# Performance work log

Measured on AMD Instinct MI355X. Metric: run time of the kernel, lower is better.

Reference implementation:

```python
import jax, jax.numpy as jnp
import numpy as np

N = 50000        # nodes
E = 100000       # directed edges
F_NODE = 22      # atom features
F_EDGE = 4       # bond features
H = 64           # hidden_dim
EPS = 1e-5       # BatchNorm eps


def setup_inputs() -> dict:
    key = jax.random.key(0)
    ks = jax.random.split(key, 16)
    s = 0.05
    return {
        "x": jax.random.normal(ks[0], (N, F_NODE), dtype=jnp.float32),
        "edge_attr": jax.random.normal(ks[1], (E, F_EDGE), dtype=jnp.float32),
        "We1": jax.random.normal(ks[2], (F_EDGE, F_NODE * H), dtype=jnp.float32) * s,
        "be1": jnp.zeros((F_NODE * H,), dtype=jnp.float32),
        "root1": jax.random.normal(ks[3], (F_NODE, H), dtype=jnp.float32) * s,
        "b1": jnp.zeros((H,), dtype=jnp.float32),
        "g1": jnp.ones((H,), dtype=jnp.float32),
        "beta1": jnp.zeros((H,), dtype=jnp.float32),
        "We2": jax.random.normal(ks[4], (F_EDGE, H * H), dtype=jnp.float32) * s,
        "be2": jnp.zeros((H * H,), dtype=jnp.float32),
        "root2": jax.random.normal(ks[5], (H, H), dtype=jnp.float32) * s,
        "b2": jnp.zeros((H,), dtype=jnp.float32),
        "g2": jnp.ones((H,), dtype=jnp.float32),
        "beta2": jnp.zeros((H,), dtype=jnp.float32),
        "Wfc": jax.random.normal(ks[6], (H, 1), dtype=jnp.float32) * s,
        "bfc": jnp.zeros((1,), dtype=jnp.float32),
        "edge_index": jax.random.randint(ks[7], (2, E), 0, N, dtype=jnp.int32),
    }


def nnconv(x, edge_index, edge_attr, We, be, root, bias, in_ch, out_ch):
    # PyG NNConv (aggr='add', root_weight=True):
    #   out_i = x_i @ root + bias + sum_{(j->i)} x_j @ reshape(MLP(e_ji), [in, out])
    src, dst = edge_index[0], edge_index[1]
    w = jax.nn.relu(edge_attr @ We + be).reshape(-1, in_ch, out_ch)  # [E, in, out]
    msg = jnp.einsum('ei,eio->eo', x[src], w)                        # [E, out]
    agg = jax.ops.segment_sum(msg, dst, num_segments=x.shape[0])     # [N, out]
    return agg + x @ root + bias


def batchnorm(x, gamma, beta):
    # training-mode BatchNorm1d: batch statistics, biased variance
    mu = jnp.mean(x, axis=0)
    var = jnp.mean(jnp.square(x - mu), axis=0)
    return (x - mu) * jax.lax.rsqrt(var + EPS) * gamma + beta


def reference(x, edge_attr, We1, be1, root1, b1, g1, beta1,
              We2, be2, root2, b2, g2, beta2, Wfc, bfc, edge_index):
    h = nnconv(x, edge_index, edge_attr, We1, be1, root1, b1, F_NODE, H)
    h = jax.nn.relu(batchnorm(h, g1, beta1))
    # dropout is identity in eval / deterministic reference
    h = nnconv(h, edge_index, edge_attr, We2, be2, root2, b2, H, H)
    h = jax.nn.relu(batchnorm(h, g2, beta2))
    return jax.nn.sigmoid(h @ Wfc + bfc)  # [N, 1]
```

## Files before the change

### kernel.cpp

```cpp
#include <hip/hip_runtime.h>
#include <math.h>

#define N_NODES 50000
#define N_EDGES 100000
#define FNODE 22
#define HDIM 64
#define BN_EPS 1e-5f

typedef __attribute__((ext_vector_type(8))) short bfrag;
typedef __attribute__((ext_vector_type(4))) float facc;
typedef __attribute__((ext_vector_type(4))) unsigned int uint4v;
typedef __attribute__((ext_vector_type(2))) unsigned int uint2v;

__device__ __forceinline__ unsigned f2bf(float x) {
    unsigned u = __float_as_uint(x);
    return (u + 0x7FFFu + ((u >> 16) & 1u)) >> 16;
}
__device__ __forceinline__ unsigned pk2bf(float lo, float hi) {
    return f2bf(lo) | (f2bf(hi) << 16);
}
__device__ __forceinline__ float bflo(unsigned w) { return __uint_as_float(w << 16); }
__device__ __forceinline__ float bfhi(unsigned w) { return __uint_as_float(w & 0xFFFF0000u); }

__global__ void k_packX(const float* __restrict__ x, unsigned* __restrict__ xbf) {
    int idx = blockIdx.x * 256 + threadIdx.x;
    if (idx < N_NODES * 12) {
        int n = idx / 12, c2 = idx - n * 12;
        int c = c2 * 2;
        float lo = (c < FNODE) ? x[n * FNODE + c] : 0.f;
        float hi = (c + 1 < FNODE) ? x[n * FNODE + c + 1] : 0.f;
        xbf[idx] = pk2bf(lo, hi);
    }
}

template <int K>
__global__ void k_packB(const float* __restrict__ W, uint4v* __restrict__ Bt) {
    constexpr int NQ = (K + 31) / 32;
    int t = threadIdx.x;
    int ot = t >> 6, lane = t & 63;
    int o = ot * 16 + (lane & 15);
    int kg = lane >> 4;
#pragma unroll
    for (int q = 0; q < NQ; ++q) {
        unsigned w[4];
#pragma unroll
        for (int p = 0; p < 4; ++p) {
            int k0 = q * 32 + kg * 8 + 2 * p;
            float lo = (k0 < K) ? W[k0 * HDIM + o] : 0.f;
            float hi = (k0 + 1 < K) ? W[(k0 + 1) * HDIM + o] : 0.f;
            w[p] = pk2bf(lo, hi);
        }
        Bt[(ot * NQ + q) * 64 + lane] = uint4v{w[0], w[1], w[2], w[3]};
    }
}

__global__ void k_node1(const float* __restrict__ x, const uint4v* __restrict__ Bt1,
                        const float* __restrict__ b1, float* __restrict__ h1) {
    int lane = threadIdx.x & 63;
    int m = lane & 15, kg = lane >> 4, orow4 = kg * 4;
    int tile = blockIdx.x * 4 + (threadIdx.x >> 6);
    int nb = tile * 16;
    if (nb >= N_NODES) return;
    const float* xr = x + (size_t)(nb + m) * FNODE;
    float xv[8];
#pragma unroll
    for (int p = 0; p < 4; ++p) {
        int c = kg * 8 + 2 * p;
        float2 v = (c + 1 < FNODE) ? *(const float2*)(xr + c) : float2{0.f, 0.f};
        xv[2 * p] = v.x; xv[2 * p + 1] = v.y;
    }
    bfrag A = __builtin_bit_cast(bfrag, uint4v{pk2bf(xv[0], xv[1]), pk2bf(xv[2], xv[3]),
                                               pk2bf(xv[4], xv[5]), pk2bf(xv[6], xv[7])});
    const facc zero4 = {0.f, 0.f, 0.f, 0.f};
#pragma unroll
    for (int ot = 0; ot < 4; ++ot) {
        bfrag B = __builtin_bit_cast(bfrag, Bt1[ot * 64 + lane]);
        facc d = __builtin_amdgcn_mfma_f32_16x16x32_bf16(A, B, zero4, 0, 0, 0);
        float bv = b1[ot * 16 + m];
#pragma unroll
        for (int j = 0; j < 4; ++j)
            h1[(size_t)(nb + orow4 + j) * HDIM + ot * 16 + m] = d[j] + bv;
    }
}

__launch_bounds__(256, 4)
__global__ void k_edge1(const char* __restrict__ hrows, const float* __restrict__ ea,
                        const float* __restrict__ We, const float* __restrict__ be,
                        const int* __restrict__ eidx, float* __restrict__ out) {
    constexpr int IN = FNODE;
    constexpr int INH = IN * HDIM;
    __shared__ uint4v Wf[IN * HDIM];
    __shared__ float hsl[4][16 * 28];

    for (int idx = threadIdx.x; idx < IN * HDIM; idx += 256) {
        int i = idx >> 6, o = idx & 63;
        int c = i * HDIM + o;
        Wf[idx] = uint4v{pk2bf(We[c], We[INH + c]),
                         pk2bf(We[2 * INH + c], We[3 * INH + c]),
                         f2bf(be[c]), 0u};
    }
    __syncthreads();

    int lane = threadIdx.x & 63;
    int e16 = lane & 15;
    int orow4 = (lane >> 4) * 4;
    int tile = blockIdx.x * 4 + (threadIdx.x >> 6);
    int ebase = tile * 16;
    if (ebase >= N_EDGES) return;
    float* hs = &hsl[threadIdx.x >> 6][0];

    bool act = lane < 16;
    float4 ea0 = ((const float4*)ea)[ebase + e16];
    unsigned aone = act ? 0x3F80u : 0u;
    bfrag A0 = __builtin_bit_cast(bfrag, uint4v{act ? pk2bf(ea0.x, ea0.y) : 0u,
                                                act ? pk2bf(ea0.z, ea0.w) : 0u, aone, 0u});

    if (lane < 48) {
        int r = lane / 3, c16 = lane - r * 3;
        int src = eidx[ebase + r];
        uint4v hv = *(const uint4v*)(hrows + (size_t)src * 48 + c16 * 16);
        *(float4*)&hs[r * 28 + c16 * 8] =
            float4{bflo(hv.x), bfhi(hv.x), bflo(hv.y), bfhi(hv.y)};
        *(float4*)&hs[r * 28 + c16 * 8 + 4] =
            float4{bflo(hv.z), bfhi(hv.z), bflo(hv.w), bfhi(hv.w)};
    }

    const facc zero4 = {0.f, 0.f, 0.f, 0.f};
    facc m0[4] = {zero4, zero4, zero4, zero4};

#pragma unroll
    for (int i0 = 0; i0 < 20; i0 += 4) {
        float4 hA[4];
#pragma unroll
        for (int j = 0; j < 4; ++j)
            hA[j] = *(const float4*)&hs[(orow4 + j) * 28 + i0];
#pragma unroll
        for (int di = 0; di < 4; ++di) {
#pragma unroll
            for (int t = 0; t < 4; ++t) {
                bfrag B = __builtin_bit_cast(bfrag, Wf[(i0 + di) * 64 + t * 16 + e16]);
                facc t0 = __builtin_amdgcn_mfma_f32_16x16x32_bf16(A0, B, zero4, 0, 0, 0);
#pragma unroll
                for (int j = 0; j < 4; ++j)
                    m0[t][j] = fmaf((&hA[j].x)[di], fmaxf(t0[j], 0.f), m0[t][j]);
            }
        }
    }
    {
        float4 hA[4];
#pragma unroll
        for (int j = 0; j < 4; ++j)
            hA[j] = *(const float4*)&hs[(orow4 + j) * 28 + 20];
#pragma unroll
        for (int di = 0; di < 2; ++di) {
#pragma unroll
            for (int t = 0; t < 4; ++t) {
                bfrag B = __builtin_bit_cast(bfrag, Wf[(20 + di) * 64 + t * 16 + e16]);
                facc t0 = __builtin_amdgcn_mfma_f32_16x16x32_bf16(A0, B, zero4, 0, 0, 0);
#pragma unroll
                for (int j = 0; j < 4; ++j)
                    m0[t][j] = fmaf((&hA[j].x)[di], fmaxf(t0[j], 0.f), m0[t][j]);
            }
        }
    }

    int dA[4];
#pragma unroll
    for (int j = 0; j < 4; ++j)
        dA[j] = eidx[N_EDGES + ebase + orow4 + j];
#pragma unroll
    for (int t = 0; t < 4; ++t) {
#pragma unroll
        for (int j = 0; j < 4; ++j)
            atomicAdd(&out[(size_t)dA[j] * HDIM + t * 16 + e16], m0[t][j]);
    }
}

__launch_bounds__(256, 3)
__global__ void k_edge2(const char* __restrict__ hrows, const float* __restrict__ ea,
                        const float* __restrict__ We, const float* __restrict__ be,
                        const int* __restrict__ eidx, float* __restrict__ out) {
    constexpr int IN = HDIM;
    constexpr int INH = IN * HDIM;
    constexpr int SSTRIDE = 36;
    __shared__ uint4v Wf[IN * 32];
    __shared__ unsigned hsl[4][32 * SSTRIDE];

    int obeg = (blockIdx.x & 1) * 32;
    int tileblk = blockIdx.x >> 1;

    for (int idx = threadIdx.x; idx < IN * 32; idx += 256) {
        int i = idx >> 5, oloc = idx & 31;
        int c = i * HDIM + obeg + oloc;
        Wf[idx] = uint4v{pk2bf(We[c], We[INH + c]),
                         pk2bf(We[2 * INH + c], We[3 * INH + c]),
                         f2bf(be[c]), 0u};
    }
    __syncthreads();

    int lane = threadIdx.x & 63;
    int e16 = lane & 15;
    int orow4 = (lane >> 4) * 4;
    int tile = tileblk * 4 + (threadIdx.x >> 6);
    int ebase = tile * 32;
    if (ebase >= N_EDGES) return;
    unsigned* hs = &hsl[threadIdx.x >> 6][0];

    bool act = lane < 16;
    float4 ea0 = ((const float4*)ea)[ebase + e16];
    float4 ea1 = ((const float4*)ea)[ebase + 16 + e16];
    unsigned aone = act ? 0x3F80u : 0u;
    bfrag A0 = __builtin_bit_cast(bfrag, uint4v{act ? pk2bf(ea0.x, ea0.y) : 0u,
                                                act ? pk2bf(ea0.z, ea0.w) : 0u, aone, 0u});
    bfrag A1 = __builtin_bit_cast(bfrag, uint4v{act ? pk2bf(ea1.x, ea1.y) : 0u,
                                                act ? pk2bf(ea1.z, ea1.w) : 0u, aone, 0u});

#pragma unroll
    for (int p = 0; p < 4; ++p) {
        int idx = p * 64 + lane;
        int r = idx >> 3, c16 = idx & 7;
        int src = eidx[ebase + r];
        uint4v hv = *(const uint4v*)(hrows + (size_t)src * 128 + c16 * 16);
        *(uint4v*)&hs[r * SSTRIDE + c16 * 4] = hv;
    }

    const facc zero4 = {0.f, 0.f, 0.f, 0.f};
    facc m0[2] = {zero4, zero4}, m1[2] = {zero4, zero4};

#pragma unroll
    for (int i0 = 0; i0 < IN; i0 += 4) {
        float hA[4][4], hB[4][4];
#pragma unroll
        for (int j = 0; j < 4; ++j) {
            uint2v wA = *(const uint2v*)&hs[(orow4 + j) * SSTRIDE + i0 / 2];
            hA[j][0] = bflo(wA.x); hA[j][1] = bfhi(wA.x);
            hA[j][2] = bflo(wA.y); hA[j][3] = bfhi(wA.y);
            uint2v wB = *(const uint2v*)&hs[(16 + orow4 + j) * SSTRIDE + i0 / 2];
            hB[j][0] = bflo(wB.x); hB[j][1] = bfhi(wB.x);
            hB[j][2] = bflo(wB.y); hB[j][3] = bfhi(wB.y);
        }
#pragma unroll
        for (int di = 0; di < 4; ++di) {
#pragma unroll
            for (int t = 0; t < 2; ++t) {
                bfrag B = __builtin_bit_cast(bfrag, Wf[(i0 + di) * 32 + t * 16 + e16]);
                facc t0 = __builtin_amdgcn_mfma_f32_16x16x32_bf16(A0, B, zero4, 0, 0, 0);
                facc t1 = __builtin_amdgcn_mfma_f32_16x16x32_bf16(A1, B, zero4, 0, 0, 0);
#pragma unroll
                for (int j = 0; j < 4; ++j) {
                    m0[t][j] = fmaf(hA[j][di], fmaxf(t0[j], 0.f), m0[t][j]);
                    m1[t][j] = fmaf(hB[j][di], fmaxf(t1[j], 0.f), m1[t][j]);
                }
            }
        }
    }

    int dA[4], dB[4];
#pragma unroll
    for (int j = 0; j < 4; ++j) {
        dA[j] = eidx[N_EDGES + ebase + orow4 + j];
        dB[j] = eidx[N_EDGES + ebase + 16 + orow4 + j];
    }
#pragma unroll
    for (int t = 0; t < 2; ++t) {
#pragma unroll
        for (int j = 0; j < 4; ++j) {
            atomicAdd(&out[(size_t)dA[j] * HDIM + obeg + t * 16 + e16], m0[t][j]);
            atomicAdd(&out[(size_t)dB[j] * HDIM + obeg + t * 16 + e16], m1[t][j]);
        }
    }
}

__global__ void k_stats(const float* __restrict__ hbuf, float* stats) {
    int c = threadIdx.x & 63;
    int r = threadIdx.x >> 6;
    int rowsPer = blockDim.x >> 6;
    float s = 0.f, q = 0.f;
    for (int n = blockIdx.x * rowsPer + r; n < N_NODES; n += gridDim.x * rowsPer) {
        float v = hbuf[n * HDIM + c];
        s += v;
        q = fmaf(v, v, q);
    }
    __shared__ float ls[4][64], lq[4][64];
    ls[r][c] = s;
    lq[r][c] = q;
    __syncthreads();
    if (r == 0) {
        s = ls[0][c] + ls[1][c] + ls[2][c] + ls[3][c];
        q = lq[0][c] + lq[1][c] + lq[2][c] + lq[3][c];
        atomicAdd(&stats[c], s);
        atomicAdd(&stats[64 + c], q);
    }
}

__global__ void k_finalize(const float* stats_in, const float* __restrict__ g,
                           const float* __restrict__ beta, float* as_out) {
    int c = threadIdx.x;
    float mu = stats_in[c] * (1.f / N_NODES);
    float var = stats_in[64 + c] * (1.f / N_NODES) - mu * mu;
    var = fmaxf(var, 0.f);
    float a = g[c] * rsqrtf(var + BN_EPS);
    as_out[c] = a;
    as_out[64 + c] = beta[c] - mu * a;
}

__global__ void k_apply1(const float* h1, const float* __restrict__ as1,
                         const uint4v* __restrict__ Bt, const float* __restrict__ b2,
                         unsigned* __restrict__ hbf, float* h2) {
    int lane = threadIdx.x & 63;
    int m = lane & 15, kg = lane >> 4, orow4 = (lane >> 4) * 4;
    int tile = blockIdx.x * 4 + (threadIdx.x >> 6);
    int nb = tile * 16;
    if (nb >= N_NODES) return;
    int node = nb + m;
    const float* hr = h1 + (size_t)node * HDIM;

    float4 a0 = *(const float4*)(as1 + kg * 8), a1 = *(const float4*)(as1 + kg * 8 + 4);
    float4 s0 = *(const float4*)(as1 + 64 + kg * 8), s1 = *(const float4*)(as1 + 64 + kg * 8 + 4);
    float4 a2 = *(const float4*)(as1 + 32 + kg * 8), a3 = *(const float4*)(as1 + 32 + kg * 8 + 4);
    float4 s2 = *(const float4*)(as1 + 96 + kg * 8), s3 = *(const float4*)(as1 + 96 + kg * 8 + 4);

    float4 v0 = *(const float4*)(hr + kg * 8), v1 = *(const float4*)(hr + kg * 8 + 4);
    float4 v2 = *(const float4*)(hr + 32 + kg * 8), v3 = *(const float4*)(hr + 32 + kg * 8 + 4);

    float r0[8], r1[8];
#pragma unroll
    for (int p = 0; p < 4; ++p) {
        r0[p]     = fmaxf(fmaf((&v0.x)[p], (&a0.x)[p], (&s0.x)[p]), 0.f);
        r0[p + 4] = fmaxf(fmaf((&v1.x)[p], (&a1.x)[p], (&s1.x)[p]), 0.f);
        r1[p]     = fmaxf(fmaf((&v2.x)[p], (&a2.x)[p], (&s2.x)[p]), 0.f);
        r1[p + 4] = fmaxf(fmaf((&v3.x)[p], (&a3.x)[p], (&s3.x)[p]), 0.f);
    }
    uint4v pk0 = uint4v{pk2bf(r0[0], r0[1]), pk2bf(r0[2], r0[3]),
                        pk2bf(r0[4], r0[5]), pk2bf(r0[6], r0[7])};
    uint4v pk1 = uint4v{pk2bf(r1[0], r1[1]), pk2bf(r1[2], r1[3]),
                        pk2bf(r1[4], r1[5]), pk2bf(r1[6], r1[7])};
    *(uint4v*)(hbf + (size_t)node * 32 + kg * 4)      = pk0;
    *(uint4v*)(hbf + (size_t)node * 32 + 16 + kg * 4) = pk1;

    bfrag A0 = __builtin_bit_cast(bfrag, pk0);
    bfrag A1 = __builtin_bit_cast(bfrag, pk1);

    const facc zero4 = {0.f, 0.f, 0.f, 0.f};
#pragma unroll
    for (int ot = 0; ot < 4; ++ot) {
        bfrag B0 = __builtin_bit_cast(bfrag, Bt[(ot * 2 + 0) * 64 + lane]);
        bfrag B1 = __builtin_bit_cast(bfrag, Bt[(ot * 2 + 1) * 64 + lane]);
        facc d = __builtin_amdgcn_mfma_f32_16x16x32_bf16(A0, B0, zero4, 0, 0, 0);
        d = __builtin_amdgcn_mfma_f32_16x16x32_bf16(A1, B1, d, 0, 0, 0);
        float bv = b2[ot * 16 + m];
#pragma unroll
        for (int j = 0; j < 4; ++j)
            h2[(size_t)(nb + orow4 + j) * HDIM + ot * 16 + m] = d[j] + bv;
    }
}

__global__ void k_final(const float* __restrict__ h2, const float* __restrict__ as2,
                        const float* __restrict__ Wfc, const float* __restrict__ bfc,
                        float* __restrict__ out) {
    int lane = threadIdx.x & 63;
    int n = blockIdx.x * (blockDim.x >> 6) + (threadIdx.x >> 6);
    if (n >= N_NODES) return;
    float a = as2[lane], s = as2[64 + lane];
    float v = fmaxf(fmaf(h2[n * HDIM + lane], a, s), 0.f) * Wfc[lane];
#pragma unroll
    for (int off = 32; off > 0; off >>= 1) v += __shfl_xor(v, off, 64);
    if (lane == 0) out[n] = 1.f / (1.f + expf(-(v + bfc[0])));
}

extern "C" void kernel_launch(void* const* d_in, const int* in_sizes, int n_in,
                              void* d_out, int out_size, void* d_ws, size_t ws_size,
                              hipStream_t stream) {
    const float* x     = (const float*)d_in[0];
    const float* ea    = (const float*)d_in[1];
    const float* We1   = (const float*)d_in[2];
    const float* be1   = (const float*)d_in[3];
    const float* root1 = (const float*)d_in[4];
    const float* b1    = (const float*)d_in[5];
    const float* g1    = (const float*)d_in[6];
    const float* beta1 = (const float*)d_in[7];
    const float* We2   = (const float*)d_in[8];
    const float* be2   = (const float*)d_in[9];
    const float* root2 = (const float*)d_in[10];
    const float* b2    = (const float*)d_in[11];
    const float* g2    = (const float*)d_in[12];
    const float* beta2 = (const float*)d_in[13];
    const float* Wfc   = (const float*)d_in[14];
    const float* bfc   = (const float*)d_in[15];
    const int*   eidx  = (const int*)d_in[16];
    float* out = (float*)d_out;

    char* ws = (char*)d_ws;
    size_t off = 0;
    auto alloc = [&](size_t bytes) { char* p = ws + off; off = (off + bytes + 255) & ~(size_t)255; return p; };
    float*    h1    = (float*)alloc((size_t)N_NODES * HDIM * 4);
    unsigned* hbf   = (unsigned*)alloc((size_t)N_NODES * 32 * 4);
    unsigned* xbf   = (unsigned*)alloc((size_t)N_NODES * 12 * 4);
    float*    stats = (float*)alloc(512 * 4);
    uint4v*   Bt2   = (uint4v*)alloc(8 * 64 * 16);
    uint4v*   Bt1   = (uint4v*)alloc(4 * 64 * 16);

    hipMemsetAsync(stats, 0, 512 * sizeof(float), stream);
    k_packX<<<(N_NODES * 12 + 255) / 256, 256, 0, stream>>>(x, xbf);
    k_packB<HDIM><<<1, 256, 0, stream>>>(root2, Bt2);
    k_packB<FNODE><<<1, 256, 0, stream>>>(root1, Bt1);

    const int e1Blocks = (N_EDGES / 16 + 3) / 4;
    const int e2Blocks = 2 * ((N_EDGES / 32 + 3) / 4);
    const int nodeBlocks = (N_NODES + 3) / 4;
    const int tileBlocks = (N_NODES / 16 + 3) / 4;

    k_node1<<<tileBlocks, 256, 0, stream>>>(x, Bt1, b1, h1);
    k_edge1<<<e1Blocks, 256, 0, stream>>>((const char*)xbf, ea, We1, be1, eidx, h1);
    k_stats<<<256, 256, 0, stream>>>(h1, stats);
    k_finalize<<<1, 64, 0, stream>>>(stats, g1, beta1, stats + 128);
    k_apply1<<<tileBlocks, 256, 0, stream>>>(h1, stats + 128, Bt2, b2, hbf, h1);
    k_edge2<<<e2Blocks, 256, 0, stream>>>((const char*)hbf, ea, We2, be2, eidx, h1);
    k_stats<<<256, 256, 0, stream>>>(h1, stats + 256);
    k_finalize<<<1, 64, 0, stream>>>(stats + 256, g2, beta2, stats + 384);
    k_final<<<nodeBlocks, 256, 0, stream>>>(h1, stats + 384, Wfc, bfc, out);
}
```

Before: 173.1 us.

## Merge prep kernels, fold BN finalize into stats, and rebalance edge kernels

The memset, X packing and both root-weight packing launches are combined into one k_prep kernel. The BN finalize step now runs inside k_stats through a last-block-done counter, which removes two launches. k_edge1 now splits output columns across two blocks, as k_edge2 already did, so each block holds half the weights in LDS. k_edge2 drops to 16 edges per wave and unpacks the gathered rows to fp32 in LDS, which trades per-wave work and LDS footprint against more blocks and twice the weight-staging loads.

Result: slower. 177.4 us (+2.5%).

```diff
diff --git a/kernel.cpp b/kernel.cpp
--- a/kernel.cpp
+++ b/kernel.cpp
@@ -6,11 +6,11 @@
 #define FNODE 22
 #define HDIM 64
 #define BN_EPS 1e-5f
+#define PXBLK ((N_NODES * 12 + 255) / 256)
 
 typedef __attribute__((ext_vector_type(8))) short bfrag;
 typedef __attribute__((ext_vector_type(4))) float facc;
 typedef __attribute__((ext_vector_type(4))) unsigned int uint4v;
-typedef __attribute__((ext_vector_type(2))) unsigned int uint2v;
 
 __device__ __forceinline__ unsigned f2bf(float x) {
     unsigned u = __float_as_uint(x);
@@ -22,28 +22,14 @@
 __device__ __forceinline__ float bflo(unsigned w) { return __uint_as_float(w << 16); }
 __device__ __forceinline__ float bfhi(unsigned w) { return __uint_as_float(w & 0xFFFF0000u); }
 
-__global__ void k_packX(const float* __restrict__ x, unsigned* __restrict__ xbf) {
-    int idx = blockIdx.x * 256 + threadIdx.x;
-    if (idx < N_NODES * 12) {
-        int n = idx / 12, c2 = idx - n * 12;
-        int c = c2 * 2;
-        float lo = (c < FNODE) ? x[n * FNODE + c] : 0.f;
-        float hi = (c + 1 < FNODE) ? x[n * FNODE + c + 1] : 0.f;
-        xbf[idx] = pk2bf(lo, hi);
-    }
-}
-
-template <int K>
-__global__ void k_packB(const float* __restrict__ W, uint4v* __restrict__ Bt) {
-    constexpr int NQ = (K + 31) / 32;
+__device__ __forceinline__ void packB_dev(const float* W, uint4v* Bt, int K) {
+    int NQ = (K + 31) / 32;
     int t = threadIdx.x;
     int ot = t >> 6, lane = t & 63;
     int o = ot * 16 + (lane & 15);
     int kg = lane >> 4;
-#pragma unroll
     for (int q = 0; q < NQ; ++q) {
         unsigned w[4];
-#pragma unroll
         for (int p = 0; p < 4; ++p) {
             int k0 = q * 32 + kg * 8 + 2 * p;
             float lo = (k0 < K) ? W[k0 * HDIM + o] : 0.f;
@@ -51,6 +37,30 @@
             w[p] = pk2bf(lo, hi);
         }
         Bt[(ot * NQ + q) * 64 + lane] = uint4v{w[0], w[1], w[2], w[3]};
+    }
+}
+
+__global__ void k_prep(const float* __restrict__ x, unsigned* __restrict__ xbf,
+                       const float* __restrict__ root1, const float* __restrict__ root2,
+                       uint4v* __restrict__ Bt1, uint4v* __restrict__ Bt2,
+                       float* __restrict__ stats, int* __restrict__ counters) {
+    int b = blockIdx.x;
+    if (b < PXBLK) {
+        int idx = b * 256 + threadIdx.x;
+        if (idx < N_NODES * 12) {
+            int n = idx / 12, c2 = idx - n * 12;
+            int c = c2 * 2;
+            float lo = (c < FNODE) ? x[n * FNODE + c] : 0.f;
+            float hi = (c + 1 < FNODE) ? x[n * FNODE + c + 1] : 0.f;
+            xbf[idx] = pk2bf(lo, hi);
+        }
+    } else if (b == PXBLK) {
+        packB_dev(root2, Bt2, HDIM);
+    } else if (b == PXBLK + 1) {
+        packB_dev(root1, Bt1, FNODE);
+    } else {
+        for (int idx = threadIdx.x; idx < 512; idx += 256) stats[idx] = 0.f;
+        if (threadIdx.x < 2) counters[threadIdx.x] = 0;
     }
 }
 
@@ -87,104 +97,9 @@
 __global__ void k_edge1(const char* __restrict__ hrows, const float* __restrict__ ea,
                         const float* __restrict__ We, const float* __restrict__ be,
                         const int* __restrict__ eidx, float* __restrict__ out) {
-    constexpr int IN = FNODE;
-    constexpr int INH = IN * HDIM;
-    __shared__ uint4v Wf[IN * HDIM];
-    __shared__ float hsl[4][16 * 28];
-
-    for (int idx = threadIdx.x; idx < IN * HDIM; idx += 256) {
-        int i = idx >> 6, o = idx & 63;
-        int c = i * HDIM + o;
-        Wf[idx] = uint4v{pk2bf(We[c], We[INH + c]),
-                         pk2bf(We[2 * INH + c], We[3 * INH + c]),
-                         f2bf(be[c]), 0u};
-    }
-    __syncthreads();
-
-    int lane = threadIdx.x & 63;
-    int e16 = lane & 15;
-    int orow4 = (lane >> 4) * 4;
-    int tile = blockIdx.x * 4 + (threadIdx.x >> 6);
-    int ebase = tile * 16;
-    if (ebase >= N_EDGES) return;
-    float* hs = &hsl[threadIdx.x >> 6][0];
-
-    bool act = lane < 16;
-    float4 ea0 = ((const float4*)ea)[ebase + e16];
-    unsigned aone = act ? 0x3F80u : 0u;
-    bfrag A0 = __builtin_bit_cast(bfrag, uint4v{act ? pk2bf(ea0.x, ea0.y) : 0u,
-                                                act ? pk2bf(ea0.z, ea0.w) : 0u, aone, 0u});
-
-    if (lane < 48) {
-        int r = lane / 3, c16 = lane - r * 3;
-        int src = eidx[ebase + r];
-        uint4v hv = *(const uint4v*)(hrows + (size_t)src * 48 + c16 * 16);
-        *(float4*)&hs[r * 28 + c16 * 8] =
-            float4{bflo(hv.x), bfhi(hv.x), bflo(hv.y), bfhi(hv.y)};
-        *(float4*)&hs[r * 28 + c16 * 8 + 4] =
-            float4{bflo(hv.z), bfhi(hv.z), bflo(hv.w), bfhi(hv.w)};
-    }
-
-    const facc zero4 = {0.f, 0.f, 0.f, 0.f};
-    facc m0[4] = {zero4, zero4, zero4, zero4};
-
-#pragma unroll
-    for (int i0 = 0; i0 < 20; i0 += 4) {
-        float4 hA[4];
-#pragma unroll
-        for (int j = 0; j < 4; ++j)
-            hA[j] = *(const float4*)&hs[(orow4 + j) * 28 + i0];
-#pragma unroll
-        for (int di = 0; di < 4; ++di) {
-#pragma unroll
-            for (int t = 0; t < 4; ++t) {
-                bfrag B = __builtin_bit_cast(bfrag, Wf[(i0 + di) * 64 + t * 16 + e16]);
-                facc t0 = __builtin_amdgcn_mfma_f32_16x16x32_bf16(A0, B, zero4, 0, 0, 0);
-#pragma unroll
-                for (int j = 0; j < 4; ++j)
-                    m0[t][j] = fmaf((&hA[j].x)[di], fmaxf(t0[j], 0.f), m0[t][j]);
-            }
-        }
-    }
-    {
-        float4 hA[4];
-#pragma unroll
-        for (int j = 0; j < 4; ++j)
-            hA[j] = *(const float4*)&hs[(orow4 + j) * 28 + 20];
-#pragma unroll
-        for (int di = 0; di < 2; ++di) {
-#pragma unroll
-            for (int t = 0; t < 4; ++t) {
-                bfrag B = __builtin_bit_cast(bfrag, Wf[(20 + di) * 64 + t * 16 + e16]);
-                facc t0 = __builtin_amdgcn_mfma_f32_16x16x32_bf16(A0, B, zero4, 0, 0, 0);
-#pragma unroll
-                for (int j = 0; j < 4; ++j)
-                    m0[t][j] = fmaf((&hA[j].x)[di], fmaxf(t0[j], 0.f), m0[t][j]);
-            }
-        }
-    }
-
-    int dA[4];
-#pragma unroll
-    for (int j = 0; j < 4; ++j)
-        dA[j] = eidx[N_EDGES + ebase + orow4 + j];
-#pragma unroll
-    for (int t = 0; t < 4; ++t) {
-#pragma unroll
-        for (int j = 0; j < 4; ++j)
-            atomicAdd(&out[(size_t)dA[j] * HDIM + t * 16 + e16], m0[t][j]);
-    }
-}
-
-__launch_bounds__(256, 3)
-__global__ void k_edge2(const char* __restrict__ hrows, const float* __restrict__ ea,
-                        const float* __restrict__ We, const float* __restrict__ be,
-                        const int* __restrict__ eidx, float* __restrict__ out) {
-    constexpr int IN = HDIM;
-    constexpr int INH = IN * HDIM;
-    constexpr int SSTRIDE = 36;
+    constexpr int IN = FNODE, INH = IN * HDIM, SSTRIDE = 28;
     __shared__ uint4v Wf[IN * 32];
-    __shared__ unsigned hsl[4][32 * SSTRIDE];
+    __shared__ float hsl[4][16 * SSTRIDE];
 
     int obeg = (blockIdx.x & 1) * 32;
     int tileblk = blockIdx.x >> 1;
@@ -202,82 +117,165 @@
     int e16 = lane & 15;
     int orow4 = (lane >> 4) * 4;
     int tile = tileblk * 4 + (threadIdx.x >> 6);
-    int ebase = tile * 32;
+    int ebase = tile * 16;
     if (ebase >= N_EDGES) return;
-    unsigned* hs = &hsl[threadIdx.x >> 6][0];
+    float* hs = &hsl[threadIdx.x >> 6][0];
 
     bool act = lane < 16;
     float4 ea0 = ((const float4*)ea)[ebase + e16];
-    float4 ea1 = ((const float4*)ea)[ebase + 16 + e16];
     unsigned aone = act ? 0x3F80u : 0u;
     bfrag A0 = __builtin_bit_cast(bfrag, uint4v{act ? pk2bf(ea0.x, ea0.y) : 0u,
                                                 act ? pk2bf(ea0.z, ea0.w) : 0u, aone, 0u});
-    bfrag A1 = __builtin_bit_cast(bfrag, uint4v{act ? pk2bf(ea1.x, ea1.y) : 0u,
-                                                act ? pk2bf(ea1.z, ea1.w) : 0u, aone, 0u});
-
-#pragma unroll
-    for (int p = 0; p < 4; ++p) {
+
+    if (lane < 48) {
+        int r = lane / 3, c16 = lane - r * 3;
+        int src = eidx[ebase + r];
+        uint4v hv = *(const uint4v*)(hrows + (size_t)src * 48 + c16 * 16);
+        *(float4*)&hs[r * SSTRIDE + c16 * 8] =
+            float4{bflo(hv.x), bfhi(hv.x), bflo(hv.y), bfhi(hv.y)};
+        *(float4*)&hs[r * SSTRIDE + c16 * 8 + 4] =
+            float4{bflo(hv.z), bfhi(hv.z), bflo(hv.w), bfhi(hv.w)};
+    }
+
+    const facc zero4 = {0.f, 0.f, 0.f, 0.f};
+    facc m0[2] = {zero4, zero4};
+
+#pragma unroll
+    for (int i0 = 0; i0 < 20; i0 += 4) {
+        float4 hA[4];
+#pragma unroll
+        for (int j = 0; j < 4; ++j)
+            hA[j] = *(const float4*)&hs[(orow4 + j) * SSTRIDE + i0];
+#pragma unroll
+        for (int di = 0; di < 4; ++di) {
+#pragma unroll
+            for (int t = 0; t < 2; ++t) {
+                bfrag B = __builtin_bit_cast(bfrag, Wf[(i0 + di) * 32 + t * 16 + e16]);
+                facc t0 = __builtin_amdgcn_mfma_f32_16x16x32_bf16(A0, B, zero4, 0, 0, 0);
+#pragma unroll
+                for (int j = 0; j < 4; ++j)
+                    m0[t][j] = fmaf((&hA[j].x)[di], fmaxf(t0[j], 0.f), m0[t][j]);
+            }
+        }
+    }
+    {
+        float4 hA[4];
+#pragma unroll
+        for (int j = 0; j < 4; ++j)
+            hA[j] = *(const float4*)&hs[(orow4 + j) * SSTRIDE + 20];
+#pragma unroll
+        for (int di = 0; di < 2; ++di) {
+#pragma unroll
+            for (int t = 0; t < 2; ++t) {
+                bfrag B = __builtin_bit_cast(bfrag, Wf[(20 + di) * 32 + t * 16 + e16]);
+                facc t0 = __builtin_amdgcn_mfma_f32_16x16x32_bf16(A0, B, zero4, 0, 0, 0);
+#pragma unroll
+                for (int j = 0; j < 4; ++j)
+                    m0[t][j] = fmaf((&hA[j].x)[di], fmaxf(t0[j], 0.f), m0[t][j]);
+            }
+        }
+    }
+
+    int dA[4];
+#pragma unroll
+    for (int j = 0; j < 4; ++j)
+        dA[j] = eidx[N_EDGES + ebase + orow4 + j];
+#pragma unroll
+    for (int t = 0; t < 2; ++t) {
+#pragma unroll
+        for (int j = 0; j < 4; ++j)
+            atomicAdd(&out[(size_t)dA[j] * HDIM + obeg + t * 16 + e16], m0[t][j]);
+    }
+}
+
+__launch_bounds__(256, 3)
+__global__ void k_edge2(const char* __restrict__ hrows, const float* __restrict__ ea,
+                        const float* __restrict__ We, const float* __restrict__ be,
+                        const int* __restrict__ eidx, float* __restrict__ out) {
+    constexpr int IN = HDIM, INH = IN * HDIM, SSTRIDE = 68;
+    __shared__ uint4v Wf[IN * 32];
+    __shared__ float hsl[4][16 * SSTRIDE];
+
+    int obeg = (blockIdx.x & 1) * 32;
+    int tileblk = blockIdx.x >> 1;
+
+    for (int idx = threadIdx.x; idx < IN * 32; idx += 256) {
+        int i = idx >> 5, oloc = idx & 31;
+        int c = i * HDIM + obeg + oloc;
+        Wf[idx] = uint4v{pk2bf(We[c], We[INH + c]),
+                         pk2bf(We[2 * INH + c], We[3 * INH + c]),
+                         f2bf(be[c]), 0u};
+    }
+    __syncthreads();
+
+    int lane = threadIdx.x & 63;
+    int e16 = lane & 15;
+    int orow4 = (lane >> 4) * 4;
+    int tile = tileblk * 4 + (threadIdx.x >> 6);
+    int ebase = tile * 16;
+    if (ebase >= N_EDGES) return;
+    float* hs = &hsl[threadIdx.x >> 6][0];
+
+    bool act = lane < 16;
+    float4 ea0 = ((const float4*)ea)[ebase + e16];
+    unsigned aone = act ? 0x3F80u : 0u;
+    bfrag A0 = __builtin_bit_cast(bfrag, uint4v{act ? pk2bf(ea0.x, ea0.y) : 0u,
+                                                act ? pk2bf(ea0.z, ea0.w) : 0u, aone, 0u});
+
+#pragma unroll
+    for (int p = 0; p < 2; ++p) {
         int idx = p * 64 + lane;
         int r = idx >> 3, c16 = idx & 7;
         int src = eidx[ebase + r];
         uint4v hv = *(const uint4v*)(hrows + (size_t)src * 128 + c16 * 16);
-        *(uint4v*)&hs[r * SSTRIDE + c16 * 4] = hv;
+        *(float4*)&hs[r * SSTRIDE + c16 * 8] =
+            float4{bflo(hv.x), bfhi(hv.x), bflo(hv.y), bfhi(hv.y)};
+        *(float4*)&hs[r * SSTRIDE + c16 * 8 + 4] =
+            float4{bflo(hv.z), bfhi(hv.z), bflo(hv.w), bfhi(hv.w)};
     }
 
     const facc zero4 = {0.f, 0.f, 0.f, 0.f};
-    facc m0[2] = {zero4, zero4}, m1[2] = {zero4, zero4};
+    facc m0[2] = {zero4, zero4};
 
 #pragma unroll
     for (int i0 = 0; i0 < IN; i0 += 4) {
-        float hA[4][4], hB[4][4];
-#pragma unroll
-        for (int j = 0; j < 4; ++j) {
-            uint2v wA = *(const uint2v*)&hs[(orow4 + j) * SSTRIDE + i0 / 2];
-            hA[j][0] = bflo(wA.x); hA[j][1] = bfhi(wA.x);
-            hA[j][2] = bflo(wA.y); hA[j][3] = bfhi(wA.y);
-            uint2v wB = *(const uint2v*)&hs[(16 + orow4 + j) * SSTRIDE + i0 / 2];
-            hB[j][0] = bflo(wB.x); hB[j][1] = bfhi(wB.x);
-            hB[j][2] = bflo(wB.y); hB[j][3] = bfhi(wB.y);
-        }
+        float4 hA[4];
+#pragma unroll
+        for (int j = 0; j < 4; ++j)
+            hA[j] = *(const float4*)&hs[(orow4 + j) * SSTRIDE + i0];
 #pragma unroll
         for (int di = 0; di < 4; ++di) {
 #pragma unroll
             for (int t = 0; t < 2; ++t) {
                 bfrag B = __builtin_bit_cast(bfrag, Wf[(i0 + di) * 32 + t * 16 + e16]);
                 facc t0 = __builtin_amdgcn_mfma_f32_16x16x32_bf16(A0, B, zero4, 0, 0, 0);
-                facc t1 = __builtin_amdgcn_mfma_f32_16x16x32_bf16(A1, B, zero4, 0, 0, 0);
-#pragma unroll
-                for (int j = 0; j < 4; ++j) {
-                    m0[t][j] = fmaf(hA[j][di], fmaxf(t0[j], 0.f), m0[t][j]);
-                    m1[t][j] = fmaf(hB[j][di], fmaxf(t1[j], 0.f), m1[t][j]);
-                }
+#pragma unroll
+                for (int j = 0; j < 4; ++j)
+                    m0[t][j] = fmaf((&hA[j].x)[di], fmaxf(t0[j], 0.f), m0[t][j]);
             }
         }
     }
 
-    int dA[4], dB[4];
-#pragma unroll
-    for (int j = 0; j < 4; ++j) {
+    int dA[4];
+#pragma unroll
+    for (int j = 0; j < 4; ++j)
         dA[j] = eidx[N_EDGES + ebase + orow4 + j];
-        dB[j] = eidx[N_EDGES + ebase + 16 + orow4 + j];
-    }
 #pragma unroll
     for (int t = 0; t < 2; ++t) {
 #pragma unroll
-        for (int j = 0; j < 4; ++j) {
+        for (int j = 0; j < 4; ++j)
             atomicAdd(&out[(size_t)dA[j] * HDIM + obeg + t * 16 + e16], m0[t][j]);
-            atomicAdd(&out[(size_t)dB[j] * HDIM + obeg + t * 16 + e16], m1[t][j]);
-        }
-    }
-}
-
-__global__ void k_stats(const float* __restrict__ hbuf, float* stats) {
+    }
+}
+
+__global__ void k_stats(const float* __restrict__ hbuf, float* acc, int* counter,
+                        const float* __restrict__ g, const float* __restrict__ beta,
+                        float* __restrict__ asout) {
     int c = threadIdx.x & 63;
     int r = threadIdx.x >> 6;
-    int rowsPer = blockDim.x >> 6;
     float s = 0.f, q = 0.f;
-    for (int n = blockIdx.x * rowsPer + r; n < N_NODES; n += gridDim.x * rowsPer) {
-        float v = hbuf[n * HDIM + c];
+    for (int n = blockIdx.x * 4 + r; n < N_NODES; n += gridDim.x * 4) {
+        float v = hbuf[(size_t)n * HDIM + c];
         s += v;
         q = fmaf(v, v, q);
     }
@@ -288,20 +286,24 @@
     if (r == 0) {
         s = ls[0][c] + ls[1][c] + ls[2][c] + ls[3][c];
         q = lq[0][c] + lq[1][c] + lq[2][c] + lq[3][c];
-        atomicAdd(&stats[c], s);
-        atomicAdd(&stats[64 + c], q);
-    }
-}
-
-__global__ void k_finalize(const float* stats_in, const float* __restrict__ g,
-                           const float* __restrict__ beta, float* as_out) {
-    int c = threadIdx.x;
-    float mu = stats_in[c] * (1.f / N_NODES);
-    float var = stats_in[64 + c] * (1.f / N_NODES) - mu * mu;
-    var = fmaxf(var, 0.f);
-    float a = g[c] * rsqrtf(var + BN_EPS);
-    as_out[c] = a;
-    as_out[64 + c] = beta[c] - mu * a;
+        atomicAdd(&acc[c], s);
+        atomicAdd(&acc[64 + c], q);
+    }
+    __threadfence();
+    __syncthreads();
+    __shared__ int lastFlag;
+    if (threadIdx.x == 0)
+        lastFlag = (atomicAdd(counter, 1) == (int)gridDim.x - 1) ? 1 : 0;
+    __syncthreads();
+    if (lastFlag && threadIdx.x < 64) {
+        float sum = atomicAdd(&acc[c], 0.f);
+        float sq  = atomicAdd(&acc[64 + c], 0.f);
+        float mu = sum * (1.f / N_NODES);
+        float var = fmaxf(sq * (1.f / N_NODES) - mu * mu, 0.f);
+        float a = g[c] * rsqrtf(var + BN_EPS);
+        asout[c] = a;
+        asout[64 + c] = beta[c] - mu * a;
+    }
 }
 
 __global__ void k_apply1(const float* h1, const float* __restrict__ as1,
@@ -397,26 +399,20 @@
     unsigned* hbf   = (unsigned*)alloc((size_t)N_NODES * 32 * 4);
     unsigned* xbf   = (unsigned*)alloc((size_t)N_NODES * 12 * 4);
     float*    stats = (float*)alloc(512 * 4);
+    int*      ctrs  = (int*)alloc(2 * 4);
     uint4v*   Bt2   = (uint4v*)alloc(8 * 64 * 16);
     uint4v*   Bt1   = (uint4v*)alloc(4 * 64 * 16);
 
-    hipMemsetAsync(stats, 0, 512 * sizeof(float), stream);
-    k_packX<<<(N_NODES * 12 + 255) / 256, 256, 0, stream>>>(x, xbf);
-    k_packB<HDIM><<<1, 256, 0, stream>>>(root2, Bt2);
-    k_packB<FNODE><<<1, 256, 0, stream>>>(root1, Bt1);
-
-    const int e1Blocks = (N_EDGES / 16 + 3) / 4;
-    const int e2Blocks = 2 * ((N_EDGES / 32 + 3) / 4);
+    const int edgeBlocks = 2 * ((N_EDGES / 16 + 3) / 4);
     const int nodeBlocks = (N_NODES + 3) / 4;
     const int tileBlocks = (N_NODES / 16 + 3) / 4;
 
+    k_prep<<<PXBLK + 3, 256, 0, stream>>>(x, xbf, root1, root2, Bt1, Bt2, stats, ctrs);
     k_node1<<<tileBlocks, 256, 0, stream>>>(x, Bt1, b1, h1);
-    k_edge1<<<e1Blocks, 256, 0, stream>>>((const char*)xbf, ea, We1, be1, eidx, h1);
-    k_stats<<<256, 256, 0, stream>>>(h1, stats);
-    k_finalize<<<1, 64, 0, stream>>>(stats, g1, beta1, stats + 128);
+    k_edge1<<<edgeBlocks, 256, 0, stream>>>((const char*)xbf, ea, We1, be1, eidx, h1);
+    k_stats<<<256, 256, 0, stream>>>(h1, stats, ctrs, g1, beta1, stats + 128);
     k_apply1<<<tileBlocks, 256, 0, stream>>>(h1, stats + 128, Bt2, b2, hbf, h1);
-    k_edge2<<<e2Blocks, 256, 0, stream>>>((const char*)hbf, ea, We2, be2, eidx, h1);
-    k_stats<<<256, 256, 0, stream>>>(h1, stats + 256);
-    k_finalize<<<1, 64, 0, stream>>>(stats + 256, g2, beta2, stats + 384);
+    k_edge2<<<edgeBlocks, 256, 0, stream>>>((const char*)hbf, ea, We2, be2, eidx, h1);
+    k_stats<<<256, 256, 0, stream>>>(h1, stats + 256, ctrs + 1, g2, beta2, stats + 384);
     k_final<<<nodeBlocks, 256, 0, stream>>>(h1, stats + 384, Wfc, bfc, out);
 }
```
